# Kernel tuning notes

Measured on AMD Instinct MI355X. Metric: run time of the kernel, lower is better.

Reference implementation:

```python
import jax, jax.numpy as jnp
import numpy as np
from jax import lax

RES = [8, 12, 20, 18, 32]
C = 4            # n_features
NCELLS = 2
DOMAIN = (0.0, 1.0, 0.0, 1.0)
NPTS = 1000000


def depthwise_conv3x3(a, w):
    # a: (Ncells, C, R, R); w: (C, 1, 3, 3) depthwise (groups=C), padding=1, no bias
    return lax.conv_general_dilated(
        a, w, window_strides=(1, 1), padding='SAME',
        dimension_numbers=('NCHW', 'OIHW', 'NCHW'), feature_group_count=C)


def grid_sample_2d(feat, gx, gy):
    # Custom bilinear grid sample with per-cell half-cell offsets (offset=True).
    # feat: (Ncells, C, IH, IW); gx, gy: (N,) normalized coords in [-1, 1].
    n_cells, c, ih, iw = feat.shape
    ix = (gx + 1.0) * 0.5 * (iw - 1)          # pixel coords, align_corners=True
    iy = (gy + 1.0) * 0.5 * (ih - 1)
    off = jnp.arange(n_cells, dtype=feat.dtype) / n_cells  # staggered cells
    ix = ix[None, :] + off[:, None]            # (Ncells, N)
    iy = iy[None, :] + off[:, None]
    ix0 = jnp.floor(ix)
    iy0 = jnp.floor(iy)
    wx = ix - ix0                              # fractional weights (unclamped)
    wy = iy - iy0
    x0 = jnp.clip(ix0.astype(jnp.int32), 0, iw - 1)
    x1 = jnp.clip(ix0.astype(jnp.int32) + 1, 0, iw - 1)
    y0 = jnp.clip(iy0.astype(jnp.int32), 0, ih - 1)
    y1 = jnp.clip(iy0.astype(jnp.int32) + 1, 0, ih - 1)
    flat = feat.reshape(n_cells, c, ih * iw)

    def gather(yy, xx):
        idx = yy * iw + xx                      # (Ncells, N)
        return jnp.take_along_axis(flat, idx[:, None, :], axis=2)  # (Ncells, C, N)

    nw = gather(y0, x0)
    ne = gather(y0, x1)
    sw = gather(y1, x0)
    se = gather(y1, x1)
    w_nw = ((1 - wx) * (1 - wy))[:, None, :]
    w_ne = (wx * (1 - wy))[:, None, :]
    w_sw = ((1 - wx) * wy)[:, None, :]
    w_se = (wx * wy)[:, None, :]
    return nw * w_nw + ne * w_ne + sw * w_sw + se * w_se  # (Ncells, C, N)


def encode_level(alpha, conv_w, gx, gy):
    a = jnp.tanh(depthwise_conv3x3(alpha, conv_w))
    s = grid_sample_2d(a, gx, gy)               # (Ncells, C, N)
    return s.sum(0).T                           # (N, C) == F.sum(0).view(C,-1).t()


def setup_inputs() -> dict:
    key = jax.random.key(0)
    kx, ky, kw = jax.random.split(key, 3)
    inp = {
        'x': jax.random.uniform(kx, (NPTS, 1), dtype=jnp.float32),
        'y': jax.random.uniform(ky, (NPTS, 1), dtype=jnp.float32),
        'conv_w': jax.random.normal(kw, (C, 1, 3, 3), dtype=jnp.float32) * 0.3,
    }
    for i, r in enumerate(RES):
        inp[f'F{i}'] = jax.random.uniform(
            jax.random.fold_in(key, i + 10), (NCELLS, C, r, r),
            dtype=jnp.float32, minval=-1e-5, maxval=1e-5)
    return inp


def reference(x, y, F0, F1, F2, F3, F4, conv_w):
    x_min, x_max, y_min, y_max = DOMAIN
    gx = ((x - x_min) / (x_max - x_min)) * 2.0 - 1.0   # (N,1)
    gy = ((y - y_min) / (y_max - y_min)) * 2.0 - 1.0
    gx = gx[:, 0]
    gy = gy[:, 0]
    feats = [encode_level(F, conv_w, gx, gy) for F in (F0, F1, F2, F3, F4)]
    return jnp.concatenate(feats, axis=1)              # (N, 5*C)
```

## Files before the change

kernel.cpp:

```cpp
#include <hip/hip_runtime.h>
#include <hip/hip_fp16.h>
#include <cmath>


#define NTH 512
#define PPT 2

constexpr int TOT = 15648;
#define OFF0 0
#define OFF1 512
#define OFF2 1664
#define OFF3 4864
#define OFF4 7456

template<int R>
__device__ __forceinline__ void conv_level(const float* __restrict__ F,
                                           const float* __restrict__ w,
                                           __half* __restrict__ dst,
                                           int tid, int nth)
{
    const int n = 8 * R * R;
    for (int i = tid; i < n; i += nth) {
        int c    = i & 3;
        int pos  = i >> 2;
        int cell = (pos >= R * R) ? 1 : 0;
        int rem  = pos - cell * R * R;
        int yy   = rem / R;
        int xx   = rem - yy * R;
        const float* Fc = F + (cell * 4 + c) * R * R;
        float acc = 0.f;
#pragma unroll
        for (int ky = 0; ky < 3; ++ky) {
#pragma unroll
            for (int kx = 0; kx < 3; ++kx) {
                int sy = yy + ky - 1, sx = xx + kx - 1;
                if ((unsigned)sy < (unsigned)R && (unsigned)sx < (unsigned)R)
                    acc += w[c * 9 + ky * 3 + kx] * Fc[sy * R + sx];
            }
        }
        dst[cell * (R * R * 4) + (yy * R + xx) * 4 + c] = __float2half(tanhf(acc));
    }
}

__global__ void conv_kernel(const float* __restrict__ F0, const float* __restrict__ F1,
                            const float* __restrict__ F2, const float* __restrict__ F3,
                            const float* __restrict__ F4, const float* __restrict__ w,
                            __half* __restrict__ tab)
{
    int tid = blockIdx.x * blockDim.x + threadIdx.x;
    int nth = gridDim.x * blockDim.x;
    conv_level<8 >(F0, w, tab + OFF0, tid, nth);
    conv_level<12>(F1, w, tab + OFF1, tid, nth);
    conv_level<20>(F2, w, tab + OFF2, tid, nth);
    conv_level<18>(F3, w, tab + OFF3, tid, nth);
    conv_level<32>(F4, w, tab + OFF4, tid, nth);
}

__device__ __forceinline__ float4 corner_fetch(const __half* __restrict__ p)
{
    uint2 raw = *(const uint2*)p;
    __half2 lo = *(__half2*)&raw.x;
    __half2 hi = *(__half2*)&raw.y;
    float2 f01 = __half22float2(lo);
    float2 f23 = __half22float2(hi);
    return make_float4(f01.x, f01.y, f23.x, f23.y);
}

template<int R>
__device__ __forceinline__ float4 sample_level(const __half* __restrict__ lt,
                                               float px, float py)
{
    float fx = px * (float)(R - 1);
    float fy = py * (float)(R - 1);
    float4 acc = make_float4(0.f, 0.f, 0.f, 0.f);
#pragma unroll
    for (int cell = 0; cell < 2; ++cell) {
        float ixc = fx + 0.5f * (float)cell;
        float iyc = fy + 0.5f * (float)cell;
        float fx0 = floorf(ixc);
        float fy0 = floorf(iyc);
        float wx = ixc - fx0;
        float wy = iyc - fy0;
        int ix0 = (int)fx0;
        int iy0 = (int)fy0;
        int x0 = min(max(ix0,     0), R - 1);
        int x1 = min(max(ix0 + 1, 0), R - 1);
        int y0 = min(max(iy0,     0), R - 1);
        int y1 = min(max(iy0 + 1, 0), R - 1);
        const __half* cb = lt + cell * (R * R * 4);
        float4 nw = corner_fetch(cb + (y0 * R + x0) * 4);
        float4 ne = corner_fetch(cb + (y0 * R + x1) * 4);
        float4 sw = corner_fetch(cb + (y1 * R + x0) * 4);
        float4 se = corner_fetch(cb + (y1 * R + x1) * 4);
        float u = 1.f - wx, v = 1.f - wy;
        float wnw = u * v, wne = wx * v, wsw = u * wy, wse = wx * wy;
        acc.x = fmaf(wnw, nw.x, acc.x); acc.x = fmaf(wne, ne.x, acc.x);
        acc.x = fmaf(wsw, sw.x, acc.x); acc.x = fmaf(wse, se.x, acc.x);
        acc.y = fmaf(wnw, nw.y, acc.y); acc.y = fmaf(wne, ne.y, acc.y);
        acc.y = fmaf(wsw, sw.y, acc.y); acc.y = fmaf(wse, se.y, acc.y);
        acc.z = fmaf(wnw, nw.z, acc.z); acc.z = fmaf(wne, ne.z, acc.z);
        acc.z = fmaf(wsw, sw.z, acc.z); acc.z = fmaf(wse, se.z, acc.z);
        acc.w = fmaf(wnw, nw.w, acc.w); acc.w = fmaf(wne, ne.w, acc.w);
        acc.w = fmaf(wsw, sw.w, acc.w); acc.w = fmaf(wse, se.w, acc.w);
    }
    return acc;
}

__device__ __forceinline__ void sample_body(const __half* lds,
                                            const float* __restrict__ x,
                                            const float* __restrict__ y,
                                            float* __restrict__ out, int npts)
{
    int p0 = blockIdx.x * (NTH * PPT) + threadIdx.x;
    float pxs[PPT], pys[PPT];
#pragma unroll
    for (int k = 0; k < PPT; ++k) {
        int p = p0 + k * NTH;
        int pc = (p < npts) ? p : 0;
        pxs[k] = x[pc];
        pys[k] = y[pc];
    }
#pragma unroll
    for (int k = 0; k < PPT; ++k) {
        int p = p0 + k * NTH;
        if (p >= npts) continue;
        float px = pxs[k];
        float py = pys[k];
        float4* op = (float4*)(out + (size_t)p * 20);
        op[0] = sample_level<8 >(lds + OFF0, px, py);
        op[1] = sample_level<12>(lds + OFF1, px, py);
        op[2] = sample_level<20>(lds + OFF2, px, py);
        op[3] = sample_level<18>(lds + OFF3, px, py);
        op[4] = sample_level<32>(lds + OFF4, px, py);
    }
}

__global__ __launch_bounds__(NTH, 8) void sample_kernel(const float* __restrict__ x,
                                                        const float* __restrict__ y,
                                                        const __half* __restrict__ tab,
                                                        float* __restrict__ out, int npts)
{
    __shared__ __align__(16) __half lds[TOT];
    const uint4* g4 = (const uint4*)tab;
    uint4* l4 = (uint4*)lds;
    for (int i = threadIdx.x; i < TOT * 2 / 16; i += NTH)
        l4[i] = g4[i];
    __syncthreads();
    sample_body(lds, x, y, out, npts);
}

__global__ __launch_bounds__(NTH, 4) void fused_kernel(const float* __restrict__ x,
                                                       const float* __restrict__ y,
                                                       const float* __restrict__ F0,
                                                       const float* __restrict__ F1,
                                                       const float* __restrict__ F2,
                                                       const float* __restrict__ F3,
                                                       const float* __restrict__ F4,
                                                       const float* __restrict__ w,
                                                       float* __restrict__ out, int npts)
{
    __shared__ __align__(16) __half lds[TOT];
    conv_level<8 >(F0, w, lds + OFF0, threadIdx.x, NTH);
    conv_level<12>(F1, w, lds + OFF1, threadIdx.x, NTH);
    conv_level<20>(F2, w, lds + OFF2, threadIdx.x, NTH);
    conv_level<18>(F3, w, lds + OFF3, threadIdx.x, NTH);
    conv_level<32>(F4, w, lds + OFF4, threadIdx.x, NTH);
    __syncthreads();
    sample_body(lds, x, y, out, npts);
}

extern "C" void kernel_launch(void* const* d_in, const int* in_sizes, int n_in,
                              void* d_out, int out_size, void* d_ws, size_t ws_size,
                              hipStream_t stream)
{
    const float* x  = (const float*)d_in[0];
    const float* y  = (const float*)d_in[1];
    const float* w  = (const float*)d_in[2];
    const float* F0 = (const float*)d_in[3];
    const float* F1 = (const float*)d_in[4];
    const float* F2 = (const float*)d_in[5];
    const float* F3 = (const float*)d_in[6];
    const float* F4 = (const float*)d_in[7];
    float* out = (float*)d_out;
    int npts = in_sizes[0];

    int nb = (npts + NTH * PPT - 1) / (NTH * PPT);

    if (ws_size >= (size_t)TOT * sizeof(__half)) {
        __half* tab = (__half*)d_ws;
        conv_kernel<<<(TOT + 255) / 256, 256, 0, stream>>>(F0, F1, F2, F3, F4, w, tab);
        sample_kernel<<<nb, NTH, 0, stream>>>(x, y, tab, out, npts);
    } else {
        fused_kernel<<<nb, NTH, 0, stream>>>(x, y, F0, F1, F2, F3, F4, w, out, npts);
    }
}
```

Measured before the change: 125.0 us.

## Fuse conv into sampling kernel with bf16-staged inputs and four points per thread

Drops the separate conv kernel plus workspace table, so every block recomputes the depthwise conv+tanh table in LDS. The raw feature grids are first staged into LDS as bf16 with coalesced loads, the per-thread conv weights are held in registers, and point coordinates are loaded before the conv to overlap latency. Points per thread go from 2 to 4, so fewer blocks share the redundant conv work. The cost is double LDS use (about 62KB per block), which lowers occupancy, plus bf16 rounding of the tiny-valued inputs, a precision risk for the conv results.

Measured after the change: 138.9 us. 1.11x slower.

```diff
diff --git a/kernel.cpp b/kernel.cpp
--- a/kernel.cpp
+++ b/kernel.cpp
@@ -4,7 +4,7 @@
 
 
 #define NTH 512
-#define PPT 2
+#define PPT 4
 
 constexpr int TOT = 15648;
 #define OFF0 0
@@ -13,21 +13,35 @@
 #define OFF3 4864
 #define OFF4 7456
 
+__device__ __forceinline__ void stage_level(const float* __restrict__ F,
+                                            unsigned short* __restrict__ dst,
+                                            int n, int tid)
+{
+    for (int i = tid; i < n; i += NTH) {
+        unsigned int u = __float_as_uint(F[i]);
+        dst[i] = (unsigned short)((u + 0x8000u) >> 16);
+    }
+}
+
+__device__ __forceinline__ float bf16_load(const unsigned short* p)
+{
+    return __uint_as_float(((unsigned int)*p) << 16);
+}
+
 template<int R>
-__device__ __forceinline__ void conv_level(const float* __restrict__ F,
-                                           const float* __restrict__ w,
-                                           __half* __restrict__ dst,
-                                           int tid, int nth)
+__device__ __forceinline__ void conv_level(const unsigned short* __restrict__ raw,
+                                           const float* __restrict__ wreg,
+                                           __half* __restrict__ dst, int tid)
 {
     const int n = 8 * R * R;
-    for (int i = tid; i < n; i += nth) {
+    for (int i = tid; i < n; i += NTH) {
         int c    = i & 3;
         int pos  = i >> 2;
         int cell = (pos >= R * R) ? 1 : 0;
         int rem  = pos - cell * R * R;
         int yy   = rem / R;
         int xx   = rem - yy * R;
-        const float* Fc = F + (cell * 4 + c) * R * R;
+        const unsigned short* Fc = raw + (cell * 4 + c) * R * R;
         float acc = 0.f;
 #pragma unroll
         for (int ky = 0; ky < 3; ++ky) {
@@ -35,25 +49,11 @@
             for (int kx = 0; kx < 3; ++kx) {
                 int sy = yy + ky - 1, sx = xx + kx - 1;
                 if ((unsigned)sy < (unsigned)R && (unsigned)sx < (unsigned)R)
-                    acc += w[c * 9 + ky * 3 + kx] * Fc[sy * R + sx];
+                    acc = fmaf(wreg[ky * 3 + kx], bf16_load(Fc + sy * R + sx), acc);
             }
         }
         dst[cell * (R * R * 4) + (yy * R + xx) * 4 + c] = __float2half(tanhf(acc));
     }
-}
-
-__global__ void conv_kernel(const float* __restrict__ F0, const float* __restrict__ F1,
-                            const float* __restrict__ F2, const float* __restrict__ F3,
-                            const float* __restrict__ F4, const float* __restrict__ w,
-                            __half* __restrict__ tab)
-{
-    int tid = blockIdx.x * blockDim.x + threadIdx.x;
-    int nth = gridDim.x * blockDim.x;
-    conv_level<8 >(F0, w, tab + OFF0, tid, nth);
-    conv_level<12>(F1, w, tab + OFF1, tid, nth);
-    conv_level<20>(F2, w, tab + OFF2, tid, nth);
-    conv_level<18>(F3, w, tab + OFF3, tid, nth);
-    conv_level<32>(F4, w, tab + OFF4, tid, nth);
 }
 
 __device__ __forceinline__ float4 corner_fetch(const __half* __restrict__ p)
@@ -106,49 +106,6 @@
     return acc;
 }
 
-__device__ __forceinline__ void sample_body(const __half* lds,
-                                            const float* __restrict__ x,
-                                            const float* __restrict__ y,
-                                            float* __restrict__ out, int npts)
-{
-    int p0 = blockIdx.x * (NTH * PPT) + threadIdx.x;
-    float pxs[PPT], pys[PPT];
-#pragma unroll
-    for (int k = 0; k < PPT; ++k) {
-        int p = p0 + k * NTH;
-        int pc = (p < npts) ? p : 0;
-        pxs[k] = x[pc];
-        pys[k] = y[pc];
-    }
-#pragma unroll
-    for (int k = 0; k < PPT; ++k) {
-        int p = p0 + k * NTH;
-        if (p >= npts) continue;
-        float px = pxs[k];
-        float py = pys[k];
-        float4* op = (float4*)(out + (size_t)p * 20);
-        op[0] = sample_level<8 >(lds + OFF0, px, py);
-        op[1] = sample_level<12>(lds + OFF1, px, py);
-        op[2] = sample_level<20>(lds + OFF2, px, py);
-        op[3] = sample_level<18>(lds + OFF3, px, py);
-        op[4] = sample_level<32>(lds + OFF4, px, py);
-    }
-}
-
-__global__ __launch_bounds__(NTH, 8) void sample_kernel(const float* __restrict__ x,
-                                                        const float* __restrict__ y,
-                                                        const __half* __restrict__ tab,
-                                                        float* __restrict__ out, int npts)
-{
-    __shared__ __align__(16) __half lds[TOT];
-    const uint4* g4 = (const uint4*)tab;
-    uint4* l4 = (uint4*)lds;
-    for (int i = threadIdx.x; i < TOT * 2 / 16; i += NTH)
-        l4[i] = g4[i];
-    __syncthreads();
-    sample_body(lds, x, y, out, npts);
-}
-
 __global__ __launch_bounds__(NTH, 4) void fused_kernel(const float* __restrict__ x,
                                                        const float* __restrict__ y,
                                                        const float* __restrict__ F0,
@@ -159,14 +116,53 @@
                                                        const float* __restrict__ w,
                                                        float* __restrict__ out, int npts)
 {
-    __shared__ __align__(16) __half lds[TOT];
-    conv_level<8 >(F0, w, lds + OFF0, threadIdx.x, NTH);
-    conv_level<12>(F1, w, lds + OFF1, threadIdx.x, NTH);
-    conv_level<20>(F2, w, lds + OFF2, threadIdx.x, NTH);
-    conv_level<18>(F3, w, lds + OFF3, threadIdx.x, NTH);
-    conv_level<32>(F4, w, lds + OFF4, threadIdx.x, NTH);
+    __shared__ __align__(16) __half        tab[TOT];
+    __shared__ __align__(16) unsigned short raw[TOT];
+    const int tid = threadIdx.x;
+
+    int p0 = blockIdx.x * (NTH * PPT) + tid;
+    float pxs[PPT], pys[PPT];
+#pragma unroll
+    for (int k = 0; k < PPT; ++k) {
+        int p = p0 + k * NTH;
+        int pc = (p < npts) ? p : 0;
+        pxs[k] = x[pc];
+        pys[k] = y[pc];
+    }
+    float wreg[9];
+    {
+        const float* wc = w + (tid & 3) * 9;
+#pragma unroll
+        for (int j = 0; j < 9; ++j) wreg[j] = wc[j];
+    }
+
+    stage_level(F0, raw + OFF0,  512, tid);
+    stage_level(F1, raw + OFF1, 1152, tid);
+    stage_level(F2, raw + OFF2, 3200, tid);
+    stage_level(F3, raw + OFF3, 2592, tid);
+    stage_level(F4, raw + OFF4, 8192, tid);
     __syncthreads();
-    sample_body(lds, x, y, out, npts);
+
+    conv_level<8 >(raw + OFF0, wreg, tab + OFF0, tid);
+    conv_level<12>(raw + OFF1, wreg, tab + OFF1, tid);
+    conv_level<20>(raw + OFF2, wreg, tab + OFF2, tid);
+    conv_level<18>(raw + OFF3, wreg, tab + OFF3, tid);
+    conv_level<32>(raw + OFF4, wreg, tab + OFF4, tid);
+    __syncthreads();
+
+#pragma unroll
+    for (int k = 0; k < PPT; ++k) {
+        int p = p0 + k * NTH;
+        if (p >= npts) continue;
+        float px = pxs[k];
+        float py = pys[k];
+        float4* op = (float4*)(out + (size_t)p * 20);
+        op[0] = sample_level<8 >(tab + OFF0, px, py);
+        op[1] = sample_level<12>(tab + OFF1, px, py);
+        op[2] = sample_level<20>(tab + OFF2, px, py);
+        op[3] = sample_level<18>(tab + OFF3, px, py);
+        op[4] = sample_level<32>(tab + OFF4, px, py);
+    }
 }
 
 extern "C" void kernel_launch(void* const* d_in, const int* in_sizes, int n_in,
@@ -185,12 +181,5 @@
     int npts = in_sizes[0];
 
     int nb = (npts + NTH * PPT - 1) / (NTH * PPT);
-
-    if (ws_size >= (size_t)TOT * sizeof(__half)) {
-        __half* tab = (__half*)d_ws;
-        conv_kernel<<<(TOT + 255) / 256, 256, 0, stream>>>(F0, F1, F2, F3, F4, w, tab);
-        sample_kernel<<<nb, NTH, 0, stream>>>(x, y, tab, out, npts);
-    } else {
-        fused_kernel<<<nb, NTH, 0, stream>>>(x, y, F0, F1, F2, F3, F4, w, out, npts);
-    }
+    fused_kernel<<<nb, NTH, 0, stream>>>(x, y, F0, F1, F2, F3, F4, w, out, npts);
 }
```
